# Performance work log

Hardware: AMD Instinct MI355X
Metric: run time of the kernel (lower is better)

Reference implementation:

```python
import jax, jax.numpy as jnp
import numpy as np

# dims (see shape_source)
N = 100000          # num_ent
E = 400000          # num edges
B = 2048            # batch of (sub, rel) queries
INIT_DIM = 100
UFD = 100           # user_fe_dim
ENT_DIM = INIT_DIM + 3 * UFD   # feature_method='concat' -> 400
H = 2               # attention heads
D = 64              # per-head dim
GCN = H * D         # gcn_dim = embed_dim = 128 (gcn_layer == 1)
NUM_REL = 50
NR2 = 2 * NUM_REL


def setup_inputs() -> dict:
    key = jax.random.key(0)
    ks = jax.random.split(key, 17)
    inp = {}
    # constructor / forward int tensors
    inp["edge_index"] = jax.random.randint(ks[0], (2, E), 0, N, dtype=jnp.int32)
    inp["edge_type"] = jax.random.randint(ks[1], (E,), 0, NR2, dtype=jnp.int32)
    inp["edge_type_p"] = jax.random.randint(ks[2], (E,), 0, NR2, dtype=jnp.int32)
    inp["ent_feature"] = jax.random.randint(ks[3], (N, 3), 0, 3, dtype=jnp.int32)
    inp["sub"] = jax.random.randint(ks[4], (B,), 0, N, dtype=jnp.int32)
    inp["rel"] = jax.random.randint(ks[5], (B,), 0, NR2, dtype=jnp.int32)
    inp["relp"] = jax.random.randint(ks[6], (B,), 0, NR2, dtype=jnp.int32)
    # learned parameters
    s = 0.02
    inp["id_embed"] = jax.random.normal(ks[7], (N, INIT_DIM), jnp.float32) * s
    inp["gender_tab"] = jax.random.normal(ks[8], (3, UFD), jnp.float32) * s
    inp["age_tab"] = jax.random.normal(ks[9], (9, UFD), jnp.float32) * s
    inp["level_tab"] = jax.random.normal(ks[10], (11, UFD), jnp.float32) * s
    inp["init_rel"] = jax.random.normal(ks[11], (NR2, ENT_DIM), jnp.float32) * s
    inp["W"] = jax.random.normal(ks[12], (ENT_DIM, H * D), jnp.float32) * 0.05
    inp["Wr"] = jax.random.normal(ks[13], (ENT_DIM, H * D), jnp.float32) * 0.05
    inp["att_src"] = jax.random.normal(ks[14], (H, D), jnp.float32) * 0.05
    inp["att_dst"] = jax.random.normal(ks[15], (H, D), jnp.float32) * 0.05
    inp["Wrel"] = jax.random.normal(ks[16], (ENT_DIM, GCN), jnp.float32) * 0.05
    return inp


def _segment_softmax(logits, seg, num_segments):
    # logits: [E, H], seg: [E] destination node ids
    m = jax.ops.segment_max(logits, seg, num_segments=num_segments)
    ex = jnp.exp(logits - m[seg])
    den = jax.ops.segment_sum(ex, seg, num_segments=num_segments)
    return ex / (den[seg] + 1e-16)


def _rghat_conv(x, rel_emb, edge_index, edge_type, W, Wr, att_src, att_dst, Wrel):
    # relational multi-head graph attention (RGHATConv)
    n = x.shape[0]
    h = (x @ W).reshape(n, H, D)                       # [N,H,D] projected nodes
    r_proj = (rel_emb @ Wr).reshape(-1, H, D)          # [R,H,D]
    src, dst = edge_index[0], edge_index[1]
    msg = h[src] + r_proj[edge_type]                   # [E,H,D] edge messages
    logits = jax.nn.leaky_relu(
        jnp.sum(msg * att_src, axis=-1) + jnp.sum(h[dst] * att_dst, axis=-1),
        negative_slope=0.2,
    )                                                  # [E,H]
    alpha = _segment_softmax(logits, dst, n)           # per-destination softmax
    out = jax.ops.segment_sum(alpha[..., None] * msg, dst, num_segments=n)
    out = jnp.tanh(out.reshape(n, H * D))              # [N,GCN]
    r_out = rel_emb @ Wrel                             # [R,GCN]
    return out, r_out


def reference(edge_index, edge_type, edge_type_p, ent_feature, sub, rel, relp,
              id_embed, gender_tab, age_tab, level_tab, init_rel,
              W, Wr, att_src, att_dst, Wrel):
    # feature_method == 'concat': gather per-node feature embeddings and concat
    x1 = gender_tab[ent_feature[:, 0]]
    x2 = age_tab[ent_feature[:, 1]]
    x3 = level_tab[ent_feature[:, 2]]
    init_embed = jnp.concatenate([id_embed, x1, x2, x3], axis=1)  # [N, ENT_DIM]
    # single conv layer (gcn_layer == 1); dropouts are identity in eval
    x, r = _rghat_conv(init_embed, init_rel, edge_index, edge_type,
                       W, Wr, att_src, att_dst, Wrel)
    sub_emb = x[sub]                                   # index_select gather
    # add_parent_rel == False -> r returned whole (relp unused)
    return (sub_emb, r, x)
```

## Files before the change

kernel.cpp:

```cpp
#include <hip/hip_runtime.h>
#include <hip/hip_bf16.h>

#define N_NODES 100000
#define E_EDGES 400000
#define B_SUB 2048
#define INIT_DIM 100
#define UFD 100
#define ENT_DIM 400
#define GCN 128
#define NR2 100
#define KPAD 416
#define NCH 13

typedef __attribute__((ext_vector_type(8))) short shortx8;
typedef __attribute__((ext_vector_type(4))) float floatx4;

#define OUT_R_OFF ((long)B_SUB * GCN)
#define OUT_X_OFF ((long)(B_SUB + NR2) * GCN)

__device__ __forceinline__ unsigned short f2b(float f) {
    unsigned u = __float_as_uint(f);
    u += 0x7fffu + ((u >> 16) & 1u);
    return (unsigned short)(u >> 16);
}
__device__ __forceinline__ unsigned pk2(float x, float y) {
    return (unsigned)f2b(x) | ((unsigned)f2b(y) << 16);
}
__device__ __forceinline__ float blo(unsigned u) { return __uint_as_float(u << 16); }
__device__ __forceinline__ float bhi(unsigned u) { return __uint_as_float(u & 0xFFFF0000u); }

__global__ void wt_kernel(const float* __restrict__ W, unsigned short* __restrict__ Wt) {
    int idx = blockIdx.x * 256 + threadIdx.x;
    int n = idx & 127, k = idx >> 7;
    unsigned short o = 0;
    if (k < ENT_DIM) o = f2b(W[(long)k * GCN + n]);
    Wt[(long)n * KPAD + k] = o;
}

__global__ void rel_kernel(const float* __restrict__ init_rel, const float* __restrict__ Wr,
                           const float* __restrict__ Wrel, const float* __restrict__ att_src,
                           unsigned* __restrict__ rp_b, float* __restrict__ rproj_att,
                           float* __restrict__ out_r) {
    int rel = blockIdx.x;
    int tx = threadIdx.x;
    __shared__ float rl[ENT_DIM];
    __shared__ float accbuf[128];
    for (int k = tx; k < ENT_DIM; k += 128) rl[k] = init_rel[(long)rel * ENT_DIM + k];
    __syncthreads();
    float acc1 = 0.f, acc2 = 0.f;
    for (int k = 0; k < ENT_DIM; ++k) {
        float v = rl[k];
        acc1 += v * Wr[(long)k * GCN + tx];
        acc2 += v * Wrel[(long)k * GCN + tx];
    }
    out_r[rel * GCN + tx] = acc2;
    accbuf[tx] = acc1;
    int head = tx >> 6, d = tx & 63;
    float v = acc1 * att_src[head * 64 + d];
    for (int off = 32; off > 0; off >>= 1) v += __shfl_down(v, off, 64);
    if (d == 0) rproj_att[rel * 2 + head] = v;
    __syncthreads();
    if (tx < 64) rp_b[rel * 64 + tx] = pk2(accbuf[tx], accbuf[tx + 64]);
}

__device__ __forceinline__ float4 load_seg(const float* __restrict__ id_embed,
                                           const float* __restrict__ gtab,
                                           const float* __restrict__ atab,
                                           const float* __restrict__ ltab,
                                           int n, int f0, int f1, int f2, int kg) {
    if (kg < 100)      return *(const float4*)&id_embed[(long)n * INIT_DIM + kg];
    else if (kg < 200) return *(const float4*)&gtab[f0 * UFD + kg - 100];
    else if (kg < 300) return *(const float4*)&atab[f1 * UFD + kg - 200];
    else if (kg < 400) return *(const float4*)&ltab[f2 * UFD + kg - 300];
    return make_float4(0.f, 0.f, 0.f, 0.f);
}

__global__ __launch_bounds__(256) void hgemm_kernel(
        const float* __restrict__ id_embed, const float* __restrict__ gtab,
        const float* __restrict__ atab, const float* __restrict__ ltab,
        const int* __restrict__ ent_feature, const unsigned short* __restrict__ Wt,
        const float* __restrict__ att_src, const float* __restrict__ att_dst,
        unsigned* __restrict__ h_b, float* __restrict__ hsrc_att, float* __restrict__ hdst_att) {
    __shared__ __align__(16) unsigned short As[64 * 40];
    __shared__ __align__(16) unsigned short Bs[128 * 40];
    __shared__ float attS[128], attD[128];
    int t = threadIdx.x;
    if (t < 128) { attS[t] = att_src[t]; attD[t] = att_dst[t]; }
    int n0 = blockIdx.x * 64;
    int row = t >> 2, seg = t & 3;
    int n = n0 + row;
    int f0 = 0, f1 = 0, f2 = 0;
    if (n < N_NODES) {
        f0 = ent_feature[n * 3];
        f1 = ent_feature[n * 3 + 1];
        f2 = ent_feature[n * 3 + 2];
    }
    int w = t >> 6, lane = t & 63, quad = lane >> 4, l16 = lane & 15;
    floatx4 acc[8];
#pragma unroll
    for (int c = 0; c < 8; ++c) acc[c] = (floatx4){0.f, 0.f, 0.f, 0.f};

    for (int ch = 0; ch < NCH; ++ch) {
        __syncthreads();
        int kg = ch * 32 + seg * 8;
        float4 va = make_float4(0.f, 0.f, 0.f, 0.f), vb = va;
        if (n < N_NODES) {
            va = load_seg(id_embed, gtab, atab, ltab, n, f0, f1, f2, kg);
            vb = load_seg(id_embed, gtab, atab, ltab, n, f0, f1, f2, kg + 4);
        }
        uint4 u;
        u.x = pk2(va.x, va.y); u.y = pk2(va.z, va.w);
        u.z = pk2(vb.x, vb.y); u.w = pk2(vb.z, vb.w);
        *(uint4*)&As[row * 40 + seg * 8] = u;
        {
            int q = t, nB = q >> 2, k0 = (q & 3) * 8;
            *(shortx8*)&Bs[nB * 40 + k0] = *(const shortx8*)&Wt[(long)nB * KPAD + ch * 32 + k0];
            q = t + 256; nB = q >> 2; k0 = (q & 3) * 8;
            *(shortx8*)&Bs[nB * 40 + k0] = *(const shortx8*)&Wt[(long)nB * KPAD + ch * 32 + k0];
        }
        __syncthreads();
        shortx8 a = *(shortx8*)&As[(w * 16 + l16) * 40 + quad * 8];
#pragma unroll
        for (int c = 0; c < 8; ++c) {
            shortx8 b = *(shortx8*)&Bs[(c * 16 + l16) * 40 + quad * 8];
            acc[c] = __builtin_amdgcn_mfma_f32_16x16x32_bf16(a, b, acc[c], 0, 0, 0);
        }
    }
    int baseRow = n0 + w * 16 + quad * 4;
#pragma unroll
    for (int i = 0; i < 4; ++i) {
        int node = baseRow + i;
        bool ok = node < N_NODES;
#pragma unroll
        for (int c = 0; c < 4; ++c)
            if (ok) h_b[(long)node * 64 + c * 16 + l16] = pk2(acc[c][i], acc[c + 4][i]);
        float s0 = 0.f, s1 = 0.f, d0 = 0.f, d1 = 0.f;
#pragma unroll
        for (int c = 0; c < 8; ++c) {
            float v = acc[c][i];
            float as_ = attS[c * 16 + l16], ad_ = attD[c * 16 + l16];
            if (c < 4) { s0 += v * as_; d0 += v * ad_; }
            else       { s1 += v * as_; d1 += v * ad_; }
        }
#pragma unroll
        for (int m = 1; m < 16; m <<= 1) {
            s0 += __shfl_xor(s0, m, 64);
            s1 += __shfl_xor(s1, m, 64);
            d0 += __shfl_xor(d0, m, 64);
            d1 += __shfl_xor(d1, m, 64);
        }
        if (ok && l16 == 0) {
            hsrc_att[node * 2] = s0; hsrc_att[node * 2 + 1] = s1;
            hdst_att[node * 2] = d0; hdst_att[node * 2 + 1] = d1;
        }
    }
}

__global__ void zero_kernel(int* __restrict__ counts) {
    int i = blockIdx.x * blockDim.x + threadIdx.x;
    if (i < N_NODES) counts[i] = 0;
}

__global__ void hist_kernel(const int* __restrict__ edge_index, int* __restrict__ counts) {
    int e = blockIdx.x * blockDim.x + threadIdx.x;
    if (e < E_EDGES) atomicAdd(&counts[edge_index[E_EDGES + e]], 1);
}

__global__ void scan1_kernel(const int* __restrict__ counts, int* __restrict__ offs,
                             int* __restrict__ bsum) {
    __shared__ int sd[256];
    int t = threadIdx.x;
    int i = blockIdx.x * 256 + t;
    int c = (i < N_NODES) ? counts[i] : 0;
    sd[t] = c;
    __syncthreads();
    for (int off = 1; off < 256; off <<= 1) {
        int v = (t >= off) ? sd[t - off] : 0;
        __syncthreads();
        sd[t] += v;
        __syncthreads();
    }
    if (i < N_NODES) offs[i] = sd[t] - c;
    if (t == 255) bsum[blockIdx.x] = sd[255];
}

__global__ void scan2_kernel(int* __restrict__ bsum, int* __restrict__ boff, int nb) {
    __shared__ int sd[512];
    int t = threadIdx.x;
    int c = (t < nb) ? bsum[t] : 0;
    sd[t] = c;
    __syncthreads();
    for (int off = 1; off < 512; off <<= 1) {
        int v = (t >= off) ? sd[t - off] : 0;
        __syncthreads();
        sd[t] += v;
        __syncthreads();
    }
    boff[t] = sd[t] - c;
}

__global__ void scan3_kernel(int* __restrict__ offs, const int* __restrict__ boff,
                             int* __restrict__ cursor) {
    int i = blockIdx.x * 256 + threadIdx.x;
    if (i < N_NODES) {
        int o = offs[i] + boff[blockIdx.x];
        offs[i] = o;
        cursor[i] = o;
    }
}

__global__ void fill_kernel(const int* __restrict__ edge_index, const int* __restrict__ edge_type,
                            int* __restrict__ cursor,
                            const float2* __restrict__ hsrc2, const float2* __restrict__ rpa2,
                            const float2* __restrict__ hdst2,
                            unsigned* __restrict__ meta_s, float2* __restrict__ exf2) {
    int e = blockIdx.x * blockDim.x + threadIdx.x;
    if (e >= E_EDGES) return;
    int src = edge_index[e];
    int dst = edge_index[E_EDGES + e];
    int et = edge_type[e];
    int pos = atomicAdd(&cursor[dst], 1);
    float2 hs = hsrc2[src];
    float2 ra = rpa2[et];
    float2 hd = hdst2[dst];
    float x0 = hs.x + ra.x + hd.x;
    float x1 = hs.y + ra.y + hd.y;
    x0 = x0 > 0.f ? x0 : 0.2f * x0;
    x1 = x1 > 0.f ? x1 : 0.2f * x1;
    meta_s[pos] = ((unsigned)et << 17) | (unsigned)src;
    exf2[pos] = make_float2(__expf(x0), __expf(x1));
}

__global__ __launch_bounds__(256) void agg_kernel(
        const int* __restrict__ offs, const int* __restrict__ counts,
        const unsigned* __restrict__ meta_s, const float2* __restrict__ exf2,
        const unsigned* __restrict__ h_b, const unsigned* __restrict__ rp_b,
        float* __restrict__ out_x) {
    int w = threadIdx.x >> 6, l = threadIdx.x & 63;
    int dst = blockIdx.x * 4 + w;
    int start = offs[dst];
    int cnt = counts[dst];
    float acc0 = 0.f, acc1 = 0.f, den0 = 0.f, den1 = 0.f;
    int j = 0;
    for (; j + 3 < cnt; j += 4) {
        int s = start + j;
        unsigned m0 = meta_s[s], m1 = meta_s[s + 1], m2 = meta_s[s + 2], m3 = meta_s[s + 3];
        float2 e0 = exf2[s], e1 = exf2[s + 1], e2 = exf2[s + 2], e3 = exf2[s + 3];
        unsigned hb0 = h_b[(long)(m0 & 0x1FFFF) * 64 + l];
        unsigned hb1 = h_b[(long)(m1 & 0x1FFFF) * 64 + l];
        unsigned hb2 = h_b[(long)(m2 & 0x1FFFF) * 64 + l];
        unsigned hb3 = h_b[(long)(m3 & 0x1FFFF) * 64 + l];
        unsigned rb0 = rp_b[(m0 >> 17) * 64 + l];
        unsigned rb1 = rp_b[(m1 >> 17) * 64 + l];
        unsigned rb2 = rp_b[(m2 >> 17) * 64 + l];
        unsigned rb3 = rp_b[(m3 >> 17) * 64 + l];
        acc0 += e0.x * (blo(hb0) + blo(rb0)) + e1.x * (blo(hb1) + blo(rb1))
              + e2.x * (blo(hb2) + blo(rb2)) + e3.x * (blo(hb3) + blo(rb3));
        acc1 += e0.y * (bhi(hb0) + bhi(rb0)) + e1.y * (bhi(hb1) + bhi(rb1))
              + e2.y * (bhi(hb2) + bhi(rb2)) + e3.y * (bhi(hb3) + bhi(rb3));
        den0 += e0.x + e1.x + e2.x + e3.x;
        den1 += e0.y + e1.y + e2.y + e3.y;
    }
    for (; j < cnt; ++j) {
        int s = start + j;
        unsigned m0 = meta_s[s];
        float2 e0 = exf2[s];
        unsigned hb = h_b[(long)(m0 & 0x1FFFF) * 64 + l];
        unsigned rb = rp_b[(m0 >> 17) * 64 + l];
        acc0 += e0.x * (blo(hb) + blo(rb));
        acc1 += e0.y * (bhi(hb) + bhi(rb));
        den0 += e0.x;
        den1 += e0.y;
    }
    float i0 = 1.0f / (den0 + 1e-16f), i1 = 1.0f / (den1 + 1e-16f);
    out_x[(long)dst * GCN + l] = tanhf(acc0 * i0);
    out_x[(long)dst * GCN + 64 + l] = tanhf(acc1 * i1);
}

__global__ void gather_kernel(const int* __restrict__ sub, const float* __restrict__ out_x,
                              float* __restrict__ out_sub) {
    int idx = blockIdx.x * blockDim.x + threadIdx.x;
    if (idx >= B_SUB * GCN) return;
    int b = idx >> 7, d = idx & 127;
    out_sub[idx] = out_x[(long)sub[b] * GCN + d];
}

extern "C" void kernel_launch(void* const* d_in, const int* in_sizes, int n_in,
                              void* d_out, int out_size, void* d_ws, size_t ws_size,
                              hipStream_t stream) {
    const int* edge_index = (const int*)d_in[0];
    const int* edge_type  = (const int*)d_in[1];
    const int* ent_feature = (const int*)d_in[3];
    const int* sub = (const int*)d_in[4];
    const float* id_embed = (const float*)d_in[7];
    const float* gtab = (const float*)d_in[8];
    const float* atab = (const float*)d_in[9];
    const float* ltab = (const float*)d_in[10];
    const float* init_rel = (const float*)d_in[11];
    const float* W = (const float*)d_in[12];
    const float* Wr = (const float*)d_in[13];
    const float* att_src = (const float*)d_in[14];
    const float* att_dst = (const float*)d_in[15];
    const float* Wrel = (const float*)d_in[16];

    char* ws = (char*)d_ws;
    unsigned* h_b = (unsigned*)ws;                          ws += (long)N_NODES * 64 * 4;
    unsigned* rp_b = (unsigned*)ws;                         ws += (long)NR2 * 64 * 4;
    float* rproj_att = (float*)ws;                          ws += NR2 * 2 * 4;
    float* hsrc_att = (float*)ws;                           ws += (long)N_NODES * 2 * 4;
    float* hdst_att = (float*)ws;                           ws += (long)N_NODES * 2 * 4;
    unsigned short* Wt = (unsigned short*)ws;               ws += (long)GCN * KPAD * 2;
    int* counts = (int*)ws;                                 ws += (long)N_NODES * 4;
    int* offs = (int*)ws;                                   ws += (long)N_NODES * 4;
    int* cursor = (int*)ws;                                 ws += (long)N_NODES * 4;
    int* bsum = (int*)ws;                                   ws += 512 * 4;
    int* boff = (int*)ws;                                   ws += 512 * 4;
    unsigned* meta_s = (unsigned*)ws;                       ws += (long)E_EDGES * 4;
    float2* exf2 = (float2*)ws;                             ws += (long)E_EDGES * 8;

    float* out = (float*)d_out;
    float* out_sub = out;
    float* out_r = out + OUT_R_OFF;
    float* out_x = out + OUT_X_OFF;

    const int NB = (N_NODES + 255) / 256;

    wt_kernel<<<(GCN * KPAD) / 256, 256, 0, stream>>>(W, Wt);
    rel_kernel<<<NR2, 128, 0, stream>>>(init_rel, Wr, Wrel, att_src, rp_b, rproj_att, out_r);
    hgemm_kernel<<<(N_NODES + 63) / 64, 256, 0, stream>>>(id_embed, gtab, atab, ltab,
                                                          ent_feature, Wt, att_src, att_dst,
                                                          h_b, hsrc_att, hdst_att);
    zero_kernel<<<NB, 256, 0, stream>>>(counts);
    hist_kernel<<<(E_EDGES + 255) / 256, 256, 0, stream>>>(edge_index, counts);
    scan1_kernel<<<NB, 256, 0, stream>>>(counts, offs, bsum);
    scan2_kernel<<<1, 512, 0, stream>>>(bsum, boff, NB);
    scan3_kernel<<<NB, 256, 0, stream>>>(offs, boff, cursor);
    fill_kernel<<<(E_EDGES + 255) / 256, 256, 0, stream>>>(edge_index, edge_type, cursor,
                                                           (const float2*)hsrc_att,
                                                           (const float2*)rproj_att,
                                                           (const float2*)hdst_att,
                                                           meta_s, exf2);
    agg_kernel<<<N_NODES / 4, 256, 0, stream>>>(offs, counts, meta_s, exf2, h_b, rp_b, out_x);
    gather_kernel<<<(B_SUB * GCN + 255) / 256, 256, 0, stream>>>(sub, out_x, out_sub);
}
```

Before: 270.6 us.

## Load MFMA operands directly from global memory and double rows per wave in hgemm

The node-projection GEMM no longer stages A and B tiles through shared memory with two barriers per K chunk. Each lane now builds its bf16 A fragment straight from the embedding and feature tables, and reads B fragments straight from the transposed weight buffer. Each wave computes two 16-row tiles that share every B fragment, so blocks cover 128 nodes instead of 64. This removes LDS traffic and synchronisation, but B is now read from global or L2 by every wave, the A loads are less coalesced (16-byte pieces spread across rows), and the doubled accumulators raise register use.

```diff
diff --git a/kernel.cpp b/kernel.cpp
--- a/kernel.cpp
+++ b/kernel.cpp
@@ -75,83 +75,89 @@
     return make_float4(0.f, 0.f, 0.f, 0.f);
 }
 
+__device__ __forceinline__ shortx8 load_a(const float* __restrict__ id_embed,
+                                          const float* __restrict__ gtab,
+                                          const float* __restrict__ atab,
+                                          const float* __restrict__ ltab,
+                                          int n, int f0, int f1, int f2, int kg, bool ok) {
+    float4 va = make_float4(0.f, 0.f, 0.f, 0.f), vb = va;
+    if (ok) {
+        va = load_seg(id_embed, gtab, atab, ltab, n, f0, f1, f2, kg);
+        vb = load_seg(id_embed, gtab, atab, ltab, n, f0, f1, f2, kg + 4);
+    }
+    uint4 u;
+    u.x = pk2(va.x, va.y); u.y = pk2(va.z, va.w);
+    u.z = pk2(vb.x, vb.y); u.w = pk2(vb.z, vb.w);
+    union { uint4 q; shortx8 s; } cv;
+    cv.q = u;
+    return cv.s;
+}
+
 __global__ __launch_bounds__(256) void hgemm_kernel(
         const float* __restrict__ id_embed, const float* __restrict__ gtab,
         const float* __restrict__ atab, const float* __restrict__ ltab,
         const int* __restrict__ ent_feature, const unsigned short* __restrict__ Wt,
         const float* __restrict__ att_src, const float* __restrict__ att_dst,
         unsigned* __restrict__ h_b, float* __restrict__ hsrc_att, float* __restrict__ hdst_att) {
-    __shared__ __align__(16) unsigned short As[64 * 40];
-    __shared__ __align__(16) unsigned short Bs[128 * 40];
     __shared__ float attS[128], attD[128];
     int t = threadIdx.x;
     if (t < 128) { attS[t] = att_src[t]; attD[t] = att_dst[t]; }
-    int n0 = blockIdx.x * 64;
-    int row = t >> 2, seg = t & 3;
-    int n = n0 + row;
-    int f0 = 0, f1 = 0, f2 = 0;
-    if (n < N_NODES) {
-        f0 = ent_feature[n * 3];
-        f1 = ent_feature[n * 3 + 1];
-        f2 = ent_feature[n * 3 + 2];
-    }
+    __syncthreads();
     int w = t >> 6, lane = t & 63, quad = lane >> 4, l16 = lane & 15;
-    floatx4 acc[8];
-#pragma unroll
-    for (int c = 0; c < 8; ++c) acc[c] = (floatx4){0.f, 0.f, 0.f, 0.f};
+    int n0 = blockIdx.x * 128;
+    int r0 = n0 + w * 32 + l16;
+    int r1 = r0 + 16;
+    bool ok0 = r0 < N_NODES, ok1 = r1 < N_NODES;
+    int f00 = 0, f01 = 0, f02 = 0, f10 = 0, f11 = 0, f12 = 0;
+    if (ok0) { f00 = ent_feature[r0 * 3]; f01 = ent_feature[r0 * 3 + 1]; f02 = ent_feature[r0 * 3 + 2]; }
+    if (ok1) { f10 = ent_feature[r1 * 3]; f11 = ent_feature[r1 * 3 + 1]; f12 = ent_feature[r1 * 3 + 2]; }
+
+    floatx4 acc[2][8];
+#pragma unroll
+    for (int i = 0; i < 2; ++i)
+#pragma unroll
+        for (int c = 0; c < 8; ++c) acc[i][c] = (floatx4){0.f, 0.f, 0.f, 0.f};
 
     for (int ch = 0; ch < NCH; ++ch) {
-        __syncthreads();
-        int kg = ch * 32 + seg * 8;
-        float4 va = make_float4(0.f, 0.f, 0.f, 0.f), vb = va;
-        if (n < N_NODES) {
-            va = load_seg(id_embed, gtab, atab, ltab, n, f0, f1, f2, kg);
-            vb = load_seg(id_embed, gtab, atab, ltab, n, f0, f1, f2, kg + 4);
+        int kg = ch * 32 + quad * 8;
+        shortx8 a0 = load_a(id_embed, gtab, atab, ltab, r0, f00, f01, f02, kg, ok0);
+        shortx8 a1 = load_a(id_embed, gtab, atab, ltab, r1, f10, f11, f12, kg, ok1);
+#pragma unroll
+        for (int c = 0; c < 8; ++c) {
+            shortx8 b = *(const shortx8*)&Wt[(long)(c * 16 + l16) * KPAD + kg];
+            acc[0][c] = __builtin_amdgcn_mfma_f32_16x16x32_bf16(a0, b, acc[0][c], 0, 0, 0);
+            acc[1][c] = __builtin_amdgcn_mfma_f32_16x16x32_bf16(a1, b, acc[1][c], 0, 0, 0);
         }
-        uint4 u;
-        u.x = pk2(va.x, va.y); u.y = pk2(va.z, va.w);
-        u.z = pk2(vb.x, vb.y); u.w = pk2(vb.z, vb.w);
-        *(uint4*)&As[row * 40 + seg * 8] = u;
-        {
-            int q = t, nB = q >> 2, k0 = (q & 3) * 8;
-            *(shortx8*)&Bs[nB * 40 + k0] = *(const shortx8*)&Wt[(long)nB * KPAD + ch * 32 + k0];
-            q = t + 256; nB = q >> 2; k0 = (q & 3) * 8;
-            *(shortx8*)&Bs[nB * 40 + k0] = *(const shortx8*)&Wt[(long)nB * KPAD + ch * 32 + k0];
-        }
-        __syncthreads();
-        shortx8 a = *(shortx8*)&As[(w * 16 + l16) * 40 + quad * 8];
-#pragma unroll
-        for (int c = 0; c < 8; ++c) {
-            shortx8 b = *(shortx8*)&Bs[(c * 16 + l16) * 40 + quad * 8];
-            acc[c] = __builtin_amdgcn_mfma_f32_16x16x32_bf16(a, b, acc[c], 0, 0, 0);
-        }
-    }
-    int baseRow = n0 + w * 16 + quad * 4;
-#pragma unroll
-    for (int i = 0; i < 4; ++i) {
-        int node = baseRow + i;
-        bool ok = node < N_NODES;
-#pragma unroll
-        for (int c = 0; c < 4; ++c)
-            if (ok) h_b[(long)node * 64 + c * 16 + l16] = pk2(acc[c][i], acc[c + 4][i]);
-        float s0 = 0.f, s1 = 0.f, d0 = 0.f, d1 = 0.f;
-#pragma unroll
-        for (int c = 0; c < 8; ++c) {
-            float v = acc[c][i];
-            float as_ = attS[c * 16 + l16], ad_ = attD[c * 16 + l16];
-            if (c < 4) { s0 += v * as_; d0 += v * ad_; }
-            else       { s1 += v * as_; d1 += v * ad_; }
-        }
-#pragma unroll
-        for (int m = 1; m < 16; m <<= 1) {
-            s0 += __shfl_xor(s0, m, 64);
-            s1 += __shfl_xor(s1, m, 64);
-            d0 += __shfl_xor(d0, m, 64);
-            d1 += __shfl_xor(d1, m, 64);
-        }
-        if (ok && l16 == 0) {
-            hsrc_att[node * 2] = s0; hsrc_att[node * 2 + 1] = s1;
-            hdst_att[node * 2] = d0; hdst_att[node * 2 + 1] = d1;
+    }
+#pragma unroll
+    for (int i2 = 0; i2 < 2; ++i2) {
+        int baseRow = n0 + w * 32 + i2 * 16 + quad * 4;
+#pragma unroll
+        for (int i = 0; i < 4; ++i) {
+            int node = baseRow + i;
+            bool ok = node < N_NODES;
+#pragma unroll
+            for (int c = 0; c < 4; ++c)
+                if (ok) h_b[(long)node * 64 + c * 16 + l16] = pk2(acc[i2][c][i], acc[i2][c + 4][i]);
+            float s0 = 0.f, s1 = 0.f, d0 = 0.f, d1 = 0.f;
+#pragma unroll
+            for (int c = 0; c < 8; ++c) {
+                float v = acc[i2][c][i];
+                float as_ = attS[c * 16 + l16], ad_ = attD[c * 16 + l16];
+                if (c < 4) { s0 += v * as_; d0 += v * ad_; }
+                else       { s1 += v * as_; d1 += v * ad_; }
+            }
+#pragma unroll
+            for (int m = 1; m < 16; m <<= 1) {
+                s0 += __shfl_xor(s0, m, 64);
+                s1 += __shfl_xor(s1, m, 64);
+                d0 += __shfl_xor(d0, m, 64);
+                d1 += __shfl_xor(d1, m, 64);
+            }
+            if (ok && l16 == 0) {
+                hsrc_att[node * 2] = s0; hsrc_att[node * 2 + 1] = s1;
+                hdst_att[node * 2] = d0; hdst_att[node * 2 + 1] = d1;
+            }
         }
     }
 }
@@ -327,9 +333,9 @@
 
     wt_kernel<<<(GCN * KPAD) / 256, 256, 0, stream>>>(W, Wt);
     rel_kernel<<<NR2, 128, 0, stream>>>(init_rel, Wr, Wrel, att_src, rp_b, rproj_att, out_r);
-    hgemm_kernel<<<(N_NODES + 63) / 64, 256, 0, stream>>>(id_embed, gtab, atab, ltab,
-                                                          ent_feature, Wt, att_src, att_dst,
-                                                          h_b, hsrc_att, hdst_att);
+    hgemm_kernel<<<(N_NODES + 127) / 128, 256, 0, stream>>>(id_embed, gtab, atab, ltab,
+                                                            ent_feature, Wt, att_src, att_dst,
+                                                            h_b, hsrc_att, hdst_att);
     zero_kernel<<<NB, 256, 0, stream>>>(counts);
     hist_kernel<<<(E_EDGES + 255) / 256, 256, 0, stream>>>(edge_index, counts);
     scan1_kernel<<<NB, 256, 0, stream>>>(counts, offs, bsum);
```

Measured after the change: 281.9 us. 4.1% more time.
